# Optimization experiments

Measured on AMD Instinct MI355X. Metric: run time of the kernel, lower is better.

The kernel has to match this reference:

```python
import jax, jax.numpy as jnp
import numpy as np

NEG = -1000000000.0

def setup_inputs() -> dict:
    key = jax.random.key(0)
    ks = jax.random.split(key, 6)
    B, V, F, H = 8, 4, 256, 768
    video_features = jax.random.normal(ks[0], (B, V, F, H), dtype=jnp.float32)
    video_attention_mask = jax.random.randint(ks[1], (B, V, F), 0, 2) > 0  # True = masked
    s = 1.0 / np.sqrt(H)
    Wqkv = jax.random.normal(ks[2], (3 * H, H), dtype=jnp.float32) * s
    bqkv = jax.random.normal(ks[3], (3 * H,), dtype=jnp.float32) * 0.01
    Wo = jax.random.normal(ks[4], (H, H), dtype=jnp.float32) * s
    bo = jax.random.normal(ks[5], (H,), dtype=jnp.float32) * 0.01
    return {"video_features": video_features, "video_attention_mask": video_attention_mask,
            "Wqkv": Wqkv, "bqkv": bqkv, "Wo": Wo, "bo": bo}

def reference(video_features, video_attention_mask, Wqkv, bqkv, Wo, bo):
    B, V, F, H = video_features.shape
    n_heads = 12
    head_dim = H // n_heads
    S = V * F  # total frames
    x = video_features.reshape(B, S, H)
    mask = video_attention_mask.reshape(B, S)
    # fused QKV projection (torch Linear: x @ W.T + b)
    qkv = x @ Wqkv.T + bqkv                      # [B, S, 3H]
    qkv = qkv.reshape(B, S, n_heads, 3 * head_dim).transpose(0, 2, 1, 3)  # [B, h, S, 3d]
    q, k, v = jnp.split(qkv, 3, axis=-1)         # each [B, h, S, d]
    scores = jnp.einsum('bhqd,bhkd->bhqk', q, k) / np.sqrt(head_dim)
    scores = jnp.where(mask[:, None, None, :], NEG, scores)
    attn = jax.nn.softmax(scores, axis=-1)       # dropout p=0 (eval) -> identity
    out = jnp.einsum('bhqk,bhkd->bhqd', attn, v) # [B, h, S, d]
    out = out.transpose(0, 2, 1, 3).reshape(B, S, H)
    out = out @ Wo.T + bo
    return out.reshape(B, V, F, H)
```

## Files before the change

### kernel.cpp

```cpp
#include <hip/hip_runtime.h>
#include <stdint.h>

typedef unsigned short u16;
typedef unsigned int u32;
typedef __attribute__((ext_vector_type(8))) unsigned short u16x8;
typedef __attribute__((ext_vector_type(4))) unsigned short u16x4;
typedef __attribute__((ext_vector_type(4))) float f32x4;
typedef __attribute__((ext_vector_type(16))) float f32x16;
typedef __attribute__((ext_vector_type(4))) float floatx4;
typedef __attribute__((ext_vector_type(8))) __bf16 bf16x8;


__device__ __forceinline__ u16 f2bf(float f) {
  union { float f; unsigned u; } c; c.f = f;
  unsigned r = c.u + 0x7fffu + ((c.u >> 16) & 1u);
  return (u16)(r >> 16);
}

__device__ __forceinline__ u32 packbf2(float lo, float hi) {
  return (u32)f2bf(lo) | ((u32)f2bf(hi) << 16);
}

__device__ __forceinline__ bf16x8 ld_bf8(const u16* p) {
  return __builtin_bit_cast(bf16x8, *(const u16x8*)p);
}

__device__ __forceinline__ float fexp2(float x) {
#if __has_builtin(__builtin_amdgcn_exp2f)
  return __builtin_amdgcn_exp2f(x);
#else
  float r; asm("v_exp_f32 %0, %1" : "=v"(r) : "v"(x)); return r;
#endif
}

__device__ __forceinline__ void glds16(const void* g, void* l) {
  __builtin_amdgcn_global_load_lds(
      (const __attribute__((address_space(1))) void*)g,
      (__attribute__((address_space(3))) void*)l, 16, 0, 0);
}

__global__ void convert_kernel(const float* __restrict__ x,
                               const float* __restrict__ w1,
                               const float* __restrict__ w2,
                               u16* __restrict__ xb,
                               u16* __restrict__ w1b,
                               u16* __restrict__ w2b) {
  const long NX = 6291456 / 4, NW1 = 1769472 / 4, NW2 = 589824 / 4;
  const long total = NX + NW1 + NW2;
  for (long i = (long)blockIdx.x * 256 + threadIdx.x; i < total;
       i += (long)gridDim.x * 256) {
    const float* src; u16* dst; long j;
    if (i < NX)            { src = x;  dst = xb;  j = i; }
    else if (i < NX + NW1) { src = w1; dst = w1b; j = i - NX; }
    else                   { src = w2; dst = w2b; j = i - NX - NW1; }
    floatx4 v = ((const floatx4*)src)[j];
    u16x4 o;
    o[0] = f2bf(v[0]); o[1] = f2bf(v[1]); o[2] = f2bf(v[2]); o[3] = f2bf(v[3]);
    ((u16x4*)dst)[j] = o;
  }
}

__global__ __launch_bounds__(256, 2)
void qkv_gemm(const u16* __restrict__ A, const u16* __restrict__ W,
              const float* __restrict__ bias,
              u16* __restrict__ qb, u16* __restrict__ kb, u16* __restrict__ vtb) {
  __shared__ __align__(16) u16 lA[128 * 32];
  __shared__ __align__(16) u16 lB[128 * 32];
  const int tid = threadIdx.x;
  const int lane = tid & 63, wid = tid >> 6;
  const int wm = wid >> 1, wn = wid & 1;
  const int l15 = lane & 15, l4 = lane >> 4;
  const int rowA0 = blockIdx.y * 128, rowB0 = blockIdx.x * 128;

  const u16* ga = A + (size_t)(rowA0 + wid * 32 + (lane >> 2)) * 768 + (lane & 3) * 8;
  const u16* gb = W + (size_t)(rowB0 + wid * 32 + (lane >> 2)) * 768 + (lane & 3) * 8;
  u16* la0 = lA + wid * 1024;
  u16* lb0 = lB + wid * 1024;

  f32x4 acc[4][4];
  const f32x4 vz = {0.f, 0.f, 0.f, 0.f};
#pragma unroll
  for (int i = 0; i < 4; ++i)
#pragma unroll
    for (int j = 0; j < 4; ++j) acc[i][j] = vz;

  for (int k0 = 0; k0 < 768; k0 += 32) {
    glds16(ga + k0,            la0);
    glds16(ga + k0 + 16 * 768, la0 + 512);
    glds16(gb + k0,            lb0);
    glds16(gb + k0 + 16 * 768, lb0 + 512);
    __syncthreads();
    bf16x8 af[4], bfr[4];
#pragma unroll
    for (int mi = 0; mi < 4; ++mi)
      af[mi] = ld_bf8(lA + (wm * 64 + mi * 16 + l15) * 32 + l4 * 8);
#pragma unroll
    for (int ni = 0; ni < 4; ++ni)
      bfr[ni] = ld_bf8(lB + (wn * 64 + ni * 16 + l15) * 32 + l4 * 8);
#pragma unroll
    for (int mi = 0; mi < 4; ++mi)
#pragma unroll
      for (int ni = 0; ni < 4; ++ni)
        acc[mi][ni] = __builtin_amdgcn_mfma_f32_16x16x32_bf16(
            af[mi], bfr[ni], acc[mi][ni], 0, 0, 0);
    __syncthreads();
  }

  const float QSC = 0.125f * 1.44269504088896f;
#pragma unroll
  for (int ni = 0; ni < 4; ++ni) {
    int n = rowB0 + wn * 64 + ni * 16 + l15;
    int h = n / 192;
    int r3 = n - h * 192;
    int t = r3 >> 6, dd = r3 & 63;
    float bn_ = bias[n];
#pragma unroll
    for (int mi = 0; mi < 4; ++mi) {
#pragma unroll
      for (int r = 0; r < 4; ++r) {
        int m = rowA0 + wm * 64 + mi * 16 + l4 * 4 + r;
        int b = m >> 10, s = m & 1023;
        size_t bh = (size_t)(b * 12 + h);
        float v = acc[mi][ni][r] + bn_;
        if (t == 0)
          qb[bh * 65536 + (size_t)s * 64 + dd] = f2bf(v * QSC);
        else if (t == 1)
          kb[bh * 65536 + (size_t)s * 64 + dd] = f2bf(v);
        else
          vtb[bh * 65536 + (size_t)dd * 1024 + s] = f2bf(v);
      }
    }
  }
}

__global__ __launch_bounds__(256, 3)
void attn_kernel(const u16* __restrict__ qb, const u16* __restrict__ kb,
                 const u16* __restrict__ vtb, const void* __restrict__ maskp,
                 u16* __restrict__ x2) {
  const int bh = blockIdx.x, qt = blockIdx.y;
  const int b = bh / 12, h = bh - b * 12;
  const int tid = threadIdx.x;
  const int w = tid >> 6, lane = tid & 63;
  const int l31 = lane & 31, hi = lane >> 5;

  __shared__ float mbias[1024];
  __shared__ int any_big;
  __shared__ __align__(16) u16 plds[4][32][40];
  __shared__ __align__(16) u16 kvs[16384];

  if (tid == 0) any_big = 0;
  __syncthreads();
  {
    const unsigned* mu = (const unsigned*)maskp;
    int loc = 0;
    for (int i = tid; i < 2048; i += 256)
      if (mu[i] > 1u) loc = 1;
    if (loc) atomicOr(&any_big, 1);
  }
  __syncthreads();
  const float CEXP = 23.0831206542234f;
  if (any_big) {
    const unsigned char* mb = (const unsigned char*)maskp;
    for (int i = tid; i < 1024; i += 256)
      mbias[i] = mb[b * 1024 + i] ? -100000.0f : -CEXP;
  } else {
    const int* mi_ = (const int*)maskp;
    for (int i = tid; i < 1024; i += 256)
      mbias[i] = mi_[b * 1024 + i] ? -100000.0f : -CEXP;
  }

  const size_t base = (size_t)bh * 65536;
  const int q0w = qt * 128 + w * 32;

  const int rlo = lane >> 3;
  const int cg = (lane & 7) ^ (rlo & 7);
  const int srow = w * 8 + rlo;
  const u16* kg0 = kb + base + (size_t)srow * 64 + cg * 8;
  const u16* vg0 = vtb + base + (size_t)srow * 1024 + cg * 8;
  u16* kd0 = kvs + w * 512;
  u16* vd0 = kvs + 4096 + w * 512;

  bf16x8 qf[4];
#pragma unroll
  for (int dstep = 0; dstep < 4; ++dstep)
    qf[dstep] = ld_bf8(qb + base + (size_t)(q0w + l31) * 64 + dstep * 16 + hi * 8);

  f32x16 o[2];
#pragma unroll
  for (int dh = 0; dh < 2; ++dh)
#pragma unroll
    for (int r = 0; r < 16; ++r) o[dh][r] = 0.f;
  float ps = 0.f;

  glds16(kg0, kd0);
  glds16(kg0 + 32 * 64, kd0 + 2048);
  glds16(vg0, vd0);
  glds16(vg0 + 32 * 1024, vd0 + 2048);
  __syncthreads();

  for (int kt = 0; kt < 16; ++kt) {
    const int cur = kt & 1;
    if (kt < 15) {
      const int nxt = cur ^ 1;
      glds16(kg0 + (kt + 1) * 4096, kd0 + nxt * 8192);
      glds16(kg0 + (kt + 1) * 4096 + 32 * 64, kd0 + nxt * 8192 + 2048);
      glds16(vg0 + (kt + 1) * 64, vd0 + nxt * 8192);
      glds16(vg0 + (kt + 1) * 64 + 32 * 1024, vd0 + nxt * 8192 + 2048);
    }

    const u16* Kl = kvs + cur * 8192;
    const u16* Vl = kvs + cur * 8192 + 4096;

#pragma unroll
    for (int kk = 0; kk < 2; ++kk) {
      f32x16 s;
#pragma unroll
      for (int r = 0; r < 16; ++r) s[r] = 0.f;
      const int rk = kk * 32 + l31;
      __builtin_amdgcn_s_setprio(1);
#pragma unroll
      for (int dstep = 0; dstep < 4; ++dstep) {
        bf16x8 kf = ld_bf8(Kl + rk * 64 + ((dstep * 2 + hi) ^ (rk & 7)) * 8);
        s = __builtin_amdgcn_mfma_f32_32x32x16_bf16(kf, qf[dstep], s, 0, 0, 0);
      }
      __builtin_amdgcn_s_setprio(0);
#pragma unroll
      for (int g = 0; g < 4; ++g) {
        f32x4 bv = *(const f32x4*)(mbias + kt * 64 + kk * 32 + g * 8 + hi * 4);
        float p0 = fexp2(s[g * 4 + 0] + bv[0]);
        float p1 = fexp2(s[g * 4 + 1] + bv[1]);
        float p2 = fexp2(s[g * 4 + 2] + bv[2]);
        float p3 = fexp2(s[g * 4 + 3] + bv[3]);
        ps += (p0 + p1) + (p2 + p3);
        const int colb = g * 8 + hi * 4;
        *(u32*)&plds[w][l31][colb]     = packbf2(p0, p1);
        *(u32*)&plds[w][l31][colb + 2] = packbf2(p2, p3);
      }

      __builtin_amdgcn_s_setprio(1);
#pragma unroll
      for (int t = 0; t < 2; ++t) {
        bf16x8 pf = ld_bf8(&plds[w][l31][t * 16 + hi * 8]);
#pragma unroll
        for (int dh = 0; dh < 2; ++dh) {
          const int rv = dh * 32 + l31;
          const int gv = kk * 4 + t * 2 + hi;
          bf16x8 vf = ld_bf8(Vl + rv * 64 + (gv ^ (rv & 7)) * 8);
          o[dh] = __builtin_amdgcn_mfma_f32_32x32x16_bf16(vf, pf, o[dh], 0, 0, 0);
        }
      }
      __builtin_amdgcn_s_setprio(0);
    }

    __syncthreads();
  }

  ps += __shfl_xor(ps, 32, 64);
  float inv = 1.0f / ps;

  u16* obuf = kvs + w * 2304;
#pragma unroll
  for (int dh = 0; dh < 2; ++dh)
#pragma unroll
    for (int j = 0; j < 8; ++j) {
      u32 v = packbf2(o[dh][2 * j] * inv, o[dh][2 * j + 1] * inv);
      int col = dh * 32 + 8 * (j >> 1) + 4 * hi + 2 * (j & 1);
      *(u32*)(obuf + l31 * 72 + col) = v;
    }

  {
    int row2 = lane >> 1, ch = lane & 1;
    const u16* srcp = obuf + row2 * 72 + ch * 32;
    u16x8 t0 = *(const u16x8*)(srcp);
    u16x8 t1 = *(const u16x8*)(srcp + 8);
    u16x8 t2 = *(const u16x8*)(srcp + 16);
    u16x8 t3 = *(const u16x8*)(srcp + 24);
    size_t m = (size_t)b * 1024 + qt * 128 + w * 32 + row2;
    u16* dst = x2 + m * 768 + h * 64 + ch * 32;
    *(u16x8*)dst = t0;
    *(u16x8*)(dst + 8) = t1;
    *(u16x8*)(dst + 16) = t2;
    *(u16x8*)(dst + 24) = t3;
  }
}

__global__ __launch_bounds__(256, 2)
void out_gemm(const u16* __restrict__ A, const u16* __restrict__ W,
              const float* __restrict__ bias, float* __restrict__ out) {
  __shared__ __align__(16) u16 lA[128 * 32];
  __shared__ __align__(16) u16 lB[128 * 32];
  const int tid = threadIdx.x;
  const int lane = tid & 63, wid = tid >> 6;
  const int wm = wid >> 1, wn = wid & 1;
  const int l15 = lane & 15, l4 = lane >> 4;
  const int rowA0 = blockIdx.y * 128, rowB0 = blockIdx.x * 128;

  const u16* ga = A + (size_t)(rowA0 + wid * 32 + (lane >> 2)) * 768 + (lane & 3) * 8;
  const u16* gb = W + (size_t)(rowB0 + wid * 32 + (lane >> 2)) * 768 + (lane & 3) * 8;
  u16* la0 = lA + wid * 1024;
  u16* lb0 = lB + wid * 1024;

  f32x4 acc[4][4];
  const f32x4 vz = {0.f, 0.f, 0.f, 0.f};
#pragma unroll
  for (int i = 0; i < 4; ++i)
#pragma unroll
    for (int j = 0; j < 4; ++j) acc[i][j] = vz;

  for (int k0 = 0; k0 < 768; k0 += 32) {
    glds16(ga + k0,            la0);
    glds16(ga + k0 + 16 * 768, la0 + 512);
    glds16(gb + k0,            lb0);
    glds16(gb + k0 + 16 * 768, lb0 + 512);
    __syncthreads();
    bf16x8 af[4], bfr[4];
#pragma unroll
    for (int mi = 0; mi < 4; ++mi)
      af[mi] = ld_bf8(lA + (wm * 64 + mi * 16 + l15) * 32 + l4 * 8);
#pragma unroll
    for (int ni = 0; ni < 4; ++ni)
      bfr[ni] = ld_bf8(lB + (wn * 64 + ni * 16 + l15) * 32 + l4 * 8);
#pragma unroll
    for (int mi = 0; mi < 4; ++mi)
#pragma unroll
      for (int ni = 0; ni < 4; ++ni)
        acc[mi][ni] = __builtin_amdgcn_mfma_f32_16x16x32_bf16(
            af[mi], bfr[ni], acc[mi][ni], 0, 0, 0);
    __syncthreads();
  }

#pragma unroll
  for (int ni = 0; ni < 4; ++ni) {
    int n = rowB0 + wn * 64 + ni * 16 + l15;
    float bn_ = bias[n];
#pragma unroll
    for (int mi = 0; mi < 4; ++mi)
#pragma unroll
      for (int r = 0; r < 4; ++r) {
        int m = rowA0 + wm * 64 + mi * 16 + l4 * 4 + r;
        out[(size_t)m * 768 + n] = acc[mi][ni][r] + bn_;
      }
  }
}

extern "C" void kernel_launch(void* const* d_in, const int* in_sizes, int n_in,
                              void* d_out, int out_size, void* d_ws, size_t ws_size,
                              hipStream_t stream) {
  const float* x    = (const float*)d_in[0];
  const void*  mask = d_in[1];
  const float* wqkv = (const float*)d_in[2];
  const float* bqkv = (const float*)d_in[3];
  const float* wo   = (const float*)d_in[4];
  const float* bo   = (const float*)d_in[5];
  float* out = (float*)d_out;

  u16* ws = (u16*)d_ws;
  u16* xbf   = ws;
  u16* wqkvb = ws + 6291456;
  u16* wob   = ws + 8060928;
  u16* qbuf  = ws + 8650752;
  u16* kbuf  = ws + 14942208;
  u16* vtbuf = ws + 21233664;
  u16* x2buf = ws + 27525120;

  convert_kernel<<<2048, 256, 0, stream>>>(x, wqkv, wo, xbf, wqkvb, wob);
  qkv_gemm<<<dim3(18, 64), 256, 0, stream>>>(xbf, wqkvb, bqkv, qbuf, kbuf, vtbuf);
  attn_kernel<<<dim3(96, 8), 256, 0, stream>>>(qbuf, kbuf, vtbuf, mask, x2buf);
  out_gemm<<<dim3(6, 64), 256, 0, stream>>>(x2buf, wob, bo, out);
}
```

Before: 138.1 us.

## Double GEMM K-tile to 64 with XOR-swizzled LDS layout in QKV and out GEMMs

Both projection GEMMs now stage a K-slice of 64 per iteration instead of 32. This halves the number of barrier pairs per tile and issues twice the MFMAs between syncs. The global-to-LDS load mapping writes 16-byte chunks with an XOR swizzle by row, and the fragment reads apply the matching XOR to avoid LDS bank conflicts on the 128-byte row stride. Launch bounds are raised to 3 blocks per CU, which asks for tighter register allocation while LDS use per block doubles to 32 KB.

```diff
diff --git a/kernel.cpp b/kernel.cpp
--- a/kernel.cpp
+++ b/kernel.cpp
@@ -60,22 +60,23 @@
   }
 }
 
-__global__ __launch_bounds__(256, 2)
+__global__ __launch_bounds__(256, 3)
 void qkv_gemm(const u16* __restrict__ A, const u16* __restrict__ W,
               const float* __restrict__ bias,
               u16* __restrict__ qb, u16* __restrict__ kb, u16* __restrict__ vtb) {
-  __shared__ __align__(16) u16 lA[128 * 32];
-  __shared__ __align__(16) u16 lB[128 * 32];
+  __shared__ __align__(16) u16 lA[128 * 64];
+  __shared__ __align__(16) u16 lB[128 * 64];
   const int tid = threadIdx.x;
   const int lane = tid & 63, wid = tid >> 6;
   const int wm = wid >> 1, wn = wid & 1;
   const int l15 = lane & 15, l4 = lane >> 4;
+  const int h7 = l15 & 7;
   const int rowA0 = blockIdx.y * 128, rowB0 = blockIdx.x * 128;
 
-  const u16* ga = A + (size_t)(rowA0 + wid * 32 + (lane >> 2)) * 768 + (lane & 3) * 8;
-  const u16* gb = W + (size_t)(rowB0 + wid * 32 + (lane >> 2)) * 768 + (lane & 3) * 8;
-  u16* la0 = lA + wid * 1024;
-  u16* lb0 = lB + wid * 1024;
+  const int rlo = lane >> 3;
+  const int swz = (lane & 7) ^ rlo;
+  const u16* ga = A + (size_t)(rowA0 + wid * 8 + rlo) * 768 + swz * 8;
+  const u16* gb = W + (size_t)(rowB0 + wid * 8 + rlo) * 768 + swz * 8;
 
   f32x4 acc[4][4];
   const f32x4 vz = {0.f, 0.f, 0.f, 0.f};
@@ -84,25 +85,34 @@
 #pragma unroll
     for (int j = 0; j < 4; ++j) acc[i][j] = vz;
 
-  for (int k0 = 0; k0 < 768; k0 += 32) {
-    glds16(ga + k0,            la0);
-    glds16(ga + k0 + 16 * 768, la0 + 512);
-    glds16(gb + k0,            lb0);
-    glds16(gb + k0 + 16 * 768, lb0 + 512);
-    __syncthreads();
-    bf16x8 af[4], bfr[4];
-#pragma unroll
-    for (int mi = 0; mi < 4; ++mi)
-      af[mi] = ld_bf8(lA + (wm * 64 + mi * 16 + l15) * 32 + l4 * 8);
+  for (int k0 = 0; k0 < 768; k0 += 64) {
+#pragma unroll
+    for (int j = 0; j < 4; ++j) {
+      glds16(ga + k0 + j * 32 * 768, lA + j * 2048 + wid * 512);
+      glds16(gb + k0 + j * 32 * 768, lB + j * 2048 + wid * 512);
+    }
+    __syncthreads();
+    bf16x8 af[4][2], bfr[4][2];
+#pragma unroll
+    for (int mi = 0; mi < 4; ++mi)
+#pragma unroll
+      for (int ks = 0; ks < 2; ++ks)
+        af[mi][ks] = ld_bf8(lA + (wm * 64 + mi * 16 + l15) * 64 +
+                            (((ks * 4 + l4) ^ h7) * 8));
 #pragma unroll
     for (int ni = 0; ni < 4; ++ni)
-      bfr[ni] = ld_bf8(lB + (wn * 64 + ni * 16 + l15) * 32 + l4 * 8);
+#pragma unroll
+      for (int ks = 0; ks < 2; ++ks)
+        bfr[ni][ks] = ld_bf8(lB + (wn * 64 + ni * 16 + l15) * 64 +
+                             (((ks * 4 + l4) ^ h7) * 8));
 #pragma unroll
     for (int mi = 0; mi < 4; ++mi)
 #pragma unroll
       for (int ni = 0; ni < 4; ++ni)
-        acc[mi][ni] = __builtin_amdgcn_mfma_f32_16x16x32_bf16(
-            af[mi], bfr[ni], acc[mi][ni], 0, 0, 0);
+#pragma unroll
+        for (int ks = 0; ks < 2; ++ks)
+          acc[mi][ni] = __builtin_amdgcn_mfma_f32_16x16x32_bf16(
+              af[mi][ks], bfr[ni][ks], acc[mi][ni], 0, 0, 0);
     __syncthreads();
   }
 
@@ -284,21 +294,22 @@
   }
 }
 
-__global__ __launch_bounds__(256, 2)
+__global__ __launch_bounds__(256, 3)
 void out_gemm(const u16* __restrict__ A, const u16* __restrict__ W,
               const float* __restrict__ bias, float* __restrict__ out) {
-  __shared__ __align__(16) u16 lA[128 * 32];
-  __shared__ __align__(16) u16 lB[128 * 32];
+  __shared__ __align__(16) u16 lA[128 * 64];
+  __shared__ __align__(16) u16 lB[128 * 64];
   const int tid = threadIdx.x;
   const int lane = tid & 63, wid = tid >> 6;
   const int wm = wid >> 1, wn = wid & 1;
   const int l15 = lane & 15, l4 = lane >> 4;
+  const int h7 = l15 & 7;
   const int rowA0 = blockIdx.y * 128, rowB0 = blockIdx.x * 128;
 
-  const u16* ga = A + (size_t)(rowA0 + wid * 32 + (lane >> 2)) * 768 + (lane & 3) * 8;
-  const u16* gb = W + (size_t)(rowB0 + wid * 32 + (lane >> 2)) * 768 + (lane & 3) * 8;
-  u16* la0 = lA + wid * 1024;
-  u16* lb0 = lB + wid * 1024;
+  const int rlo = lane >> 3;
+  const int swz = (lane & 7) ^ rlo;
+  const u16* ga = A + (size_t)(rowA0 + wid * 8 + rlo) * 768 + swz * 8;
+  const u16* gb = W + (size_t)(rowB0 + wid * 8 + rlo) * 768 + swz * 8;
 
   f32x4 acc[4][4];
   const f32x4 vz = {0.f, 0.f, 0.f, 0.f};
@@ -307,25 +318,34 @@
 #pragma unroll
     for (int j = 0; j < 4; ++j) acc[i][j] = vz;
 
-  for (int k0 = 0; k0 < 768; k0 += 32) {
-    glds16(ga + k0,            la0);
-    glds16(ga + k0 + 16 * 768, la0 + 512);
-    glds16(gb + k0,            lb0);
-    glds16(gb + k0 + 16 * 768, lb0 + 512);
-    __syncthreads();
-    bf16x8 af[4], bfr[4];
-#pragma unroll
-    for (int mi = 0; mi < 4; ++mi)
-      af[mi] = ld_bf8(lA + (wm * 64 + mi * 16 + l15) * 32 + l4 * 8);
+  for (int k0 = 0; k0 < 768; k0 += 64) {
+#pragma unroll
+    for (int j = 0; j < 4; ++j) {
+      glds16(ga + k0 + j * 32 * 768, lA + j * 2048 + wid * 512);
+      glds16(gb + k0 + j * 32 * 768, lB + j * 2048 + wid * 512);
+    }
+    __syncthreads();
+    bf16x8 af[4][2], bfr[4][2];
+#pragma unroll
+    for (int mi = 0; mi < 4; ++mi)
+#pragma unroll
+      for (int ks = 0; ks < 2; ++ks)
+        af[mi][ks] = ld_bf8(lA + (wm * 64 + mi * 16 + l15) * 64 +
+                            (((ks * 4 + l4) ^ h7) * 8));
 #pragma unroll
     for (int ni = 0; ni < 4; ++ni)
-      bfr[ni] = ld_bf8(lB + (wn * 64 + ni * 16 + l15) * 32 + l4 * 8);
+#pragma unroll
+      for (int ks = 0; ks < 2; ++ks)
+        bfr[ni][ks] = ld_bf8(lB + (wn * 64 + ni * 16 + l15) * 64 +
+                             (((ks * 4 + l4) ^ h7) * 8));
 #pragma unroll
     for (int mi = 0; mi < 4; ++mi)
 #pragma unroll
       for (int ni = 0; ni < 4; ++ni)
-        acc[mi][ni] = __builtin_amdgcn_mfma_f32_16x16x32_bf16(
-            af[mi], bfr[ni], acc[mi][ni], 0, 0, 0);
+#pragma unroll
+        for (int ks = 0; ks < 2; ++ks)
+          acc[mi][ni] = __builtin_amdgcn_mfma_f32_16x16x32_bf16(
+              af[mi][ks], bfr[ni][ks], acc[mi][ni], 0, 0, 0);
     __syncthreads();
   }
 
```

Result: faster. 133.2 us (-3.5%).
